# Kernel optimization log

Measured on AMD Instinct MI355X. Metric: run time of the kernel, lower is better.

Reference implementation:

```python
import jax, jax.numpy as jnp
import numpy as np

H = 1024      # hidden_size
I = 2048      # intermediate_size
E = 32        # num_routed_experts
B, S = 4, 2048


def setup_inputs() -> dict:
    key = jax.random.key(0)
    ks = jax.random.split(key, 8)
    scale = 0.02
    inp = {
        "hidden_states": jax.random.normal(ks[0], (B, S, H), dtype=jnp.float32),
        # router gate: stored [H, E] so logits = x @ gate_w
        "gate_w": jax.random.normal(ks[1], (H, E), dtype=jnp.float32) * scale,
        # shared SwiGLU (num_shared_experts=1), weights stored [in, out]
        "shared_gate_w": jax.random.normal(ks[2], (H, I), dtype=jnp.float32) * scale,
        "shared_up_w": jax.random.normal(ks[3], (H, I), dtype=jnp.float32) * scale,
        "shared_down_w": jax.random.normal(ks[4], (I, H), dtype=jnp.float32) * scale,
        # routed grouped SwiGLU, weights stored [E, in, out] (matches GroupedLinear)
        "routed_gate_w": jax.random.normal(ks[5], (E, H, I), dtype=jnp.float32) * scale,
        "routed_up_w": jax.random.normal(ks[6], (E, H, I), dtype=jnp.float32) * scale,
        "routed_down_w": jax.random.normal(ks[7], (E, I, H), dtype=jnp.float32) * scale,
    }
    return inp


def _grouped_mm(a, w, group_sizes):
    # a: [T, in], w: [E, in, out], group_sizes: [E] int32 -> [T, out]
    return jax.lax.ragged_dot(a, w, group_sizes)


def _swiglu(x, gw, uw, dw):
    return (jax.nn.silu(x @ gw) * (x @ uw)) @ dw


def reference(hidden_states, gate_w, shared_gate_w, shared_up_w, shared_down_w,
              routed_gate_w, routed_up_w, routed_down_w):
    b, s, h = hidden_states.shape
    x = hidden_states.reshape(-1, h)                      # [T, H]

    # ---- shared expert ----
    shared_out = _swiglu(x, shared_gate_w, shared_up_w, shared_down_w)

    # ---- router: top-1 ----
    logits = x @ gate_w                                   # [T, E]
    topk_ids = jnp.argmax(logits, axis=-1)                # [T]
    topk_val = jnp.max(logits, axis=-1)                   # [T]
    scores = jax.nn.sigmoid(topk_val)[:, None]            # [T, 1]
    xs = x * scores                                       # scale tokens by router score

    # ---- dispatch: sort tokens by expert id ----
    tokens_per_expert = jnp.zeros((E,), jnp.int32).at[topk_ids].add(1)
    order = jnp.argsort(topk_ids)                         # token ids sorted by expert
    sorted_x = xs[order]                                  # [T, H]

    # ---- grouped SwiGLU experts ----
    g = _grouped_mm(sorted_x, routed_gate_w, tokens_per_expert)   # [T, I]
    u = _grouped_mm(sorted_x, routed_up_w, tokens_per_expert)     # [T, I]
    d = _grouped_mm(jax.nn.silu(g) * u, routed_down_w, tokens_per_expert)  # [T, H]

    # ---- combine: unsort back to token order ----
    inv = jnp.argsort(order)
    routed_out = d[inv]

    return (shared_out + routed_out).reshape(b, s, h)
```

## Files before the change

### kernel.cpp

```cpp
#include <hip/hip_runtime.h>
#include <stdint.h>
#include <stddef.h>

#define TOK 8192
#define H 1024
#define IDIM 2048
#define NE 32
#define BM 128
#define BK 64
#define MAX_TILES 96
#define GUTILES (TOK / BM + MAX_TILES)
#define DNCONV_TILES 16896
#define RT_BLOCKS (TOK / 8)
#define GUCONV_TILES 33792

typedef __attribute__((ext_vector_type(8))) short short8;
typedef __attribute__((ext_vector_type(4))) float f32x4;
typedef __attribute__((ext_vector_type(4))) float float4v;
typedef __attribute__((ext_vector_type(4))) unsigned int uint4v;


__device__ __forceinline__ unsigned short f2bf(float x) {
  unsigned u = __builtin_bit_cast(unsigned, x);
  u += 0x7fffu + ((u >> 16) & 1u);
  return (unsigned short)(u >> 16);
}

__device__ __forceinline__ unsigned cvtpk(float lo, float hi) {
  unsigned r;
  asm("v_cvt_pk_bf16_f32 %0, %1, %2" : "=v"(r) : "v"(lo), "v"(hi));
  return r;
}

__device__ __forceinline__ void gll16(const void* g, void* l) {
  __builtin_amdgcn_global_load_lds(
      (const __attribute__((address_space(1))) unsigned int*)g,
      (__attribute__((address_space(3))) unsigned int*)l, 16, 0, 0);
}

__device__ __forceinline__ f32x4 mfma16(short8 a, short8 b, f32x4 c) {
  return __builtin_amdgcn_mfma_f32_16x16x32_bf16(a, b, c, 0, 0, 0);
}

__device__ __forceinline__ void tconv_tile(
    const float* __restrict__ src, unsigned short* __restrict__ dst,
    int K, int N, int k0, int n0, int tid, void* smem)
{
  float (*t)[65] = (float(*)[65])smem;
  {
    const int r = tid >> 4;
    const int c = (tid & 15) * 4;
    #pragma unroll
    for (int i = 0; i < 4; ++i) {
      float4v v = *(const float4v*)(src + (size_t)(k0 + r + i * 16) * N + (n0 + c));
      t[r + i * 16][c + 0] = v[0];
      t[r + i * 16][c + 1] = v[1];
      t[r + i * 16][c + 2] = v[2];
      t[r + i * 16][c + 3] = v[3];
    }
  }
  __syncthreads();
  {
    const int n = tid >> 2;
    const int kc = (tid & 3) * 16;
    uint4v o0, o1;
    #pragma unroll
    for (int q = 0; q < 4; ++q) {
      o0[q] = cvtpk(t[kc + 2 * q][n],     t[kc + 2 * q + 1][n]);
      o1[q] = cvtpk(t[kc + 8 + 2 * q][n], t[kc + 8 + 2 * q + 1][n]);
    }
    unsigned short* dp = dst + (size_t)(n0 + n) * K + (k0 + kc);
    *(uint4v*)dp = o0;
    *(uint4v*)(dp + 8) = o1;
  }
}


__global__ __launch_bounds__(256) void router_tconv_kernel(
    const float* __restrict__ x, const float* __restrict__ gw,
    unsigned short* __restrict__ xbf, unsigned short* __restrict__ xsbf,
    int* __restrict__ expert_id, int* __restrict__ counts,
    const float* __restrict__ sgw, const float* __restrict__ suw,
    const float* __restrict__ rgw, const float* __restrict__ ruw,
    unsigned short* __restrict__ sgwT, unsigned short* __restrict__ suwT,
    unsigned short* __restrict__ rgwT, unsigned short* __restrict__ ruwT)
{
  __shared__ char smem[41088];
  const int tid = threadIdx.x;
  const int b = blockIdx.x;

  if (b >= RT_BLOCKS) {
    const int flat = b - RT_BLOCKS;
    const float* src;
    unsigned short* dst;
    int rem;
    if (flat < 512 * NE) {
      const int e = flat >> 9; rem = flat & 511;
      src = rgw + (size_t)e * H * IDIM; dst = rgwT + (size_t)e * H * IDIM;
    } else if (flat < 1024 * NE) {
      const int e = (flat - 512 * NE) >> 9; rem = flat & 511;
      src = ruw + (size_t)e * H * IDIM; dst = ruwT + (size_t)e * H * IDIM;
    } else if (flat < 1024 * NE + 512) {
      rem = flat - 1024 * NE;
      src = sgw; dst = sgwT;
    } else {
      rem = flat - 1024 * NE - 512;
      src = suw; dst = suwT;
    }
    tconv_tile(src, dst, H, IDIM, (rem >> 5) * 64, (rem & 31) * 64, tid, smem);
    return;
  }

  float* xl = (float*)smem;
  float (*plog)[8][NE] = (float(*)[8][NE])(smem + 32768);
  float* sscore = (float*)(smem + 40960);
  const long t0 = (long)b * 8;

  const float4v* src = (const float4v*)(x + t0 * H);
  float4v* dst = (float4v*)xl;
  #pragma unroll
  for (int i = 0; i < 8; ++i) dst[tid + i * 256] = src[tid + i * 256];
  __syncthreads();

  {
    const int e = tid & 31, c = tid >> 5;
    float acc[8] = {0, 0, 0, 0, 0, 0, 0, 0};
    const float* gp = gw + (c * 128) * NE + e;
    for (int h = 0; h < 128; ++h) {
      float g = gp[h * NE];
      const float* xr = xl + (c * 128 + h);
      #pragma unroll
      for (int tk = 0; tk < 8; ++tk) acc[tk] += xr[tk * H] * g;
    }
    #pragma unroll
    for (int tk = 0; tk < 8; ++tk) plog[c][tk][e] = acc[tk];
  }
  __syncthreads();
  {
    const int e = tid & 31, tok = tid >> 5;
    float lg = 0.f;
    #pragma unroll
    for (int c = 0; c < 8; ++c) lg += plog[c][tok][e];
    float m = lg; int be = e;
    #pragma unroll
    for (int mask = 16; mask >= 1; mask >>= 1) {
      float om = __shfl_xor(m, mask);
      int   oe = __shfl_xor(be, mask);
      if (om > m || (om == m && oe < be)) { m = om; be = oe; }
    }
    if (e == 0) {
      sscore[tok] = 1.f / (1.f + __expf(-m));
      expert_id[t0 + tok] = be;
      atomicAdd(&counts[be], 1);
    }
  }
  __syncthreads();
  {
    const float sc = sscore[tid >> 5];
    const int base = (tid >> 5) * H + (tid & 31) * 32;
    #pragma unroll
    for (int i = 0; i < 4; ++i) {
      uint4v vx, vs;
      #pragma unroll
      for (int q = 0; q < 4; ++q) {
        const float a = xl[base + i * 8 + 2 * q];
        const float bq = xl[base + i * 8 + 2 * q + 1];
        vx[q] = cvtpk(a, bq);
        vs[q] = cvtpk(a * sc, bq * sc);
      }
      *(uint4v*)(xbf  + t0 * H + base + i * 8) = vx;
      *(uint4v*)(xsbf + t0 * H + base + i * 8) = vs;
    }
  }
}


__global__ void scan_kernel(const int* __restrict__ counts, int* __restrict__ offsets,
                            int* __restrict__ cursor, int* __restrict__ tile_e,
                            int* __restrict__ tile_p, int* __restrict__ n_tiles)
{
  if (threadIdx.x != 0) return;
  int off = 0, nt = 0;
  for (int e = 0; e < NE; ++e) {
    offsets[e] = off; cursor[e] = off;
    int cc = counts[e];
    for (int k = 0; k < cc; k += BM) { tile_e[nt] = e; tile_p[nt] = off + k; ++nt; }
    off += cc;
  }
  offsets[NE] = off;
  n_tiles[0] = nt;
}


__global__ __launch_bounds__(256) void perm_kernel(
    const int* __restrict__ expert_id, int* __restrict__ cursor, int* __restrict__ perm)
{
  int t = blockIdx.x * 256 + threadIdx.x;
  int e = expert_id[t];
  int pos = atomicAdd(&cursor[e], 1);
  perm[pos] = t;
}


__global__ __launch_bounds__(256, 2) void gu_kernel(
    const unsigned short* __restrict__ xbf,
    const unsigned short* __restrict__ xsbf,
    const unsigned short* __restrict__ SG, const unsigned short* __restrict__ SU,
    const unsigned short* __restrict__ RG, const unsigned short* __restrict__ RU,
    unsigned short* __restrict__ act_sh, unsigned short* __restrict__ act_rt,
    const float* __restrict__ SDW, const float* __restrict__ RDW,
    unsigned short* __restrict__ SDT, unsigned short* __restrict__ RDT,
    const int* __restrict__ perm, const int* __restrict__ tile_e,
    const int* __restrict__ tile_p, const int* __restrict__ offsets,
    const int* __restrict__ n_tiles)
{
  __shared__ char smem[49152];

  const int tid = threadIdx.x;
  const int bidy = blockIdx.y;

  if (bidy >= GUTILES) {
    const int flat = (bidy - GUTILES) * (int)gridDim.x + (int)blockIdx.x;
    const float* src;
    unsigned short* dst;
    int rem;
    if (flat < 512 * NE) {
      const int e = flat >> 9;
      rem = flat & 511;
      src = RDW + (size_t)e * IDIM * H;
      dst = RDT + (size_t)e * IDIM * H;
    } else {
      rem = flat - 512 * NE;
      src = SDW;
      dst = SDT;
    }
    tconv_tile(src, dst, IDIM, H, (rem >> 4) * 64, (rem & 15) * 64, tid, smem);
    return;
  }

  short* Al = (short*)smem;
  short* Gl = Al + BM * BK;
  short* Ul = Gl + 128 * BK;

  const int wave = tid >> 6, lane = tid & 63;
  const int wm = wave >> 1, wn = wave & 1;

  const bool routed = bidy >= (TOK / BM);
  int row0, row_end;
  const unsigned short *Gt, *Ut, *A;
  unsigned short* act;
  if (routed) {
    const int tx = bidy - TOK / BM;
    if (tx >= *n_tiles) return;
    const int e = tile_e[tx];
    row0 = tile_p[tx];
    row_end = offsets[e + 1];
    Gt = RG + (size_t)e * H * IDIM;
    Ut = RU + (size_t)e * H * IDIM;
    A = xsbf; act = act_rt;
  } else {
    row0 = bidy * BM; row_end = row0 + BM;
    Gt = SG; Ut = SU;
    A = xbf; act = act_sh;
  }
  const int n0 = blockIdx.x * 128;

  const unsigned short *asrc[4], *gsrc[4], *usrc[4];
  int soff[4];
  #pragma unroll
  for (int i = 0; i < 4; ++i) {
    const int r = wave * 32 + i * 8 + (lane >> 3);
    int p = row0 + r;
    if (routed && p >= row_end) p = row0;
    const int arow = routed ? perm[p] : p;
    const int cb = ((lane & 7) * 16) ^ ((r & 7) << 4);
    asrc[i] = A  + (size_t)arow * H + (cb >> 1);
    gsrc[i] = Gt + (size_t)(n0 + r) * H + (cb >> 1);
    usrc[i] = Ut + (size_t)(n0 + r) * H + (cb >> 1);
    soff[i] = (wave * 32 + i * 8) * BK;
  }

  f32x4 accg[4][4] = {};
  f32x4 accu[4][4] = {};

  #pragma unroll 1
  for (int kt = 0; kt < H / BK; ++kt) {
    __syncthreads();
    #pragma unroll
    for (int i = 0; i < 4; ++i) gll16(asrc[i] + kt * BK, Al + soff[i]);
    #pragma unroll
    for (int i = 0; i < 4; ++i) gll16(gsrc[i] + kt * BK, Gl + soff[i]);
    #pragma unroll
    for (int i = 0; i < 4; ++i) gll16(usrc[i] + kt * BK, Ul + soff[i]);
    __syncthreads();

    #pragma unroll
    for (int kk = 0; kk < 2; ++kk) {
      short8 af[4];
      #pragma unroll
      for (int m = 0; m < 4; ++m) {
        const int r = wm * 64 + m * 16 + (lane & 15);
        const int cb = (kk * 64 + ((lane >> 4) * 16)) ^ ((r & 7) << 4);
        af[m] = *(const short8*)((const char*)Al + r * 128 + cb);
      }
      #pragma unroll
      for (int nf = 0; nf < 4; ++nf) {
        const int n = wn * 64 + nf * 16 + (lane & 15);
        const int cb = (kk * 64 + ((lane >> 4) * 16)) ^ ((n & 7) << 4);
        short8 bg = *(const short8*)((const char*)Gl + n * 128 + cb);
        short8 bu = *(const short8*)((const char*)Ul + n * 128 + cb);
        #pragma unroll
        for (int m = 0; m < 4; ++m) {
          accg[m][nf] = mfma16(af[m], bg, accg[m][nf]);
          accu[m][nf] = mfma16(af[m], bu, accu[m][nf]);
        }
      }
    }
  }

  #pragma unroll
  for (int m = 0; m < 4; ++m)
    #pragma unroll
    for (int nf = 0; nf < 4; ++nf) {
      const int col = n0 + wn * 64 + nf * 16 + (lane & 15);
      #pragma unroll
      for (int j = 0; j < 4; ++j) {
        const int row = row0 + wm * 64 + m * 16 + ((lane >> 4) * 4) + j;
        if (routed && row >= row_end) continue;
        const float g = accg[m][nf][j];
        const float u = accu[m][nf][j];
        const float v = (g / (1.f + __expf(-g))) * u;
        act[(size_t)row * IDIM + col] = f2bf(v);
      }
    }
}


__global__ __launch_bounds__(256, 4) void dn_kernel(
    const unsigned short* __restrict__ act_sh,
    const unsigned short* __restrict__ act_rt,
    const unsigned short* __restrict__ SD, const unsigned short* __restrict__ RD,
    float* __restrict__ out, float* __restrict__ out_rt,
    const int* __restrict__ perm, const int* __restrict__ tile_e,
    const int* __restrict__ tile_p, const int* __restrict__ offsets,
    const int* __restrict__ n_tiles)
{
  __shared__ short Al[BM * BK];
  __shared__ short Dl[128 * BK];

  const int tid = threadIdx.x;
  const int wave = tid >> 6, lane = tid & 63;
  const int wm = wave >> 1, wn = wave & 1;

  const int bidy = blockIdx.y;
  const bool routed = bidy >= (TOK / BM);
  int row0, row_end;
  const unsigned short *Dt, *A;
  if (routed) {
    const int tx = bidy - TOK / BM;
    if (tx >= *n_tiles) return;
    const int e = tile_e[tx];
    row0 = tile_p[tx];
    row_end = offsets[e + 1];
    Dt = RD + (size_t)e * H * IDIM;
    A = act_rt;
  } else {
    row0 = bidy * BM; row_end = row0 + BM;
    Dt = SD;
    A = act_sh;
  }
  const int n0 = blockIdx.x * 128;

  const unsigned short *asrc[4], *dsrc[4];
  int soff[4];
  #pragma unroll
  for (int i = 0; i < 4; ++i) {
    const int r = wave * 32 + i * 8 + (lane >> 3);
    int p = row0 + r;
    if (routed && p >= row_end) p = row0;
    const int cb = ((lane & 7) * 16) ^ ((r & 7) << 4);
    asrc[i] = A  + (size_t)p * IDIM + (cb >> 1);
    dsrc[i] = Dt + (size_t)(n0 + r) * IDIM + (cb >> 1);
    soff[i] = (wave * 32 + i * 8) * BK;
  }

  f32x4 acc[4][4] = {};

  #pragma unroll 1
  for (int kt = 0; kt < IDIM / BK; ++kt) {
    __syncthreads();
    #pragma unroll
    for (int i = 0; i < 4; ++i) gll16(asrc[i] + kt * BK, Al + soff[i]);
    #pragma unroll
    for (int i = 0; i < 4; ++i) gll16(dsrc[i] + kt * BK, Dl + soff[i]);
    __syncthreads();

    #pragma unroll
    for (int kk = 0; kk < 2; ++kk) {
      short8 af[4];
      #pragma unroll
      for (int m = 0; m < 4; ++m) {
        const int r = wm * 64 + m * 16 + (lane & 15);
        const int cb = (kk * 64 + ((lane >> 4) * 16)) ^ ((r & 7) << 4);
        af[m] = *(const short8*)((const char*)Al + r * 128 + cb);
      }
      #pragma unroll
      for (int nf = 0; nf < 4; ++nf) {
        const int n = wn * 64 + nf * 16 + (lane & 15);
        const int cb = (kk * 64 + ((lane >> 4) * 16)) ^ ((n & 7) << 4);
        short8 bd = *(const short8*)((const char*)Dl + n * 128 + cb);
        #pragma unroll
        for (int m = 0; m < 4; ++m) acc[m][nf] = mfma16(af[m], bd, acc[m][nf]);
      }
    }
  }

  #pragma unroll
  for (int m = 0; m < 4; ++m)
    #pragma unroll
    for (int nf = 0; nf < 4; ++nf) {
      const int col = n0 + wn * 64 + nf * 16 + (lane & 15);
      #pragma unroll
      for (int j = 0; j < 4; ++j) {
        const int row = row0 + wm * 64 + m * 16 + ((lane >> 4) * 4) + j;
        if (routed && row >= row_end) continue;
        const float v = acc[m][nf][j];
        if (routed) {
          const int t = perm[row];
          out_rt[(size_t)t * H + col] = v;
        } else {
          out[(size_t)row * H + col] = v;
        }
      }
    }
}


__global__ __launch_bounds__(256) void combine_kernel(
    float* __restrict__ out, const float* __restrict__ out_rt)
{
  const size_t i = ((size_t)blockIdx.x * 256 + threadIdx.x) * 4;
  float4v a = *(float4v*)(out + i);
  float4v b = *(const float4v*)(out_rt + i);
  a[0] += b[0]; a[1] += b[1]; a[2] += b[2]; a[3] += b[3];
  *(float4v*)(out + i) = a;
}


extern "C" void kernel_launch(void* const* d_in, const int* in_sizes, int n_in,
                              void* d_out, int out_size, void* d_ws, size_t ws_size,
                              hipStream_t stream) {
  (void)in_sizes; (void)n_in; (void)out_size; (void)ws_size;
  const float* x      = (const float*)d_in[0];
  const float* gate_w = (const float*)d_in[1];
  const float* sgw    = (const float*)d_in[2];
  const float* suw    = (const float*)d_in[3];
  const float* sdw    = (const float*)d_in[4];
  const float* rgw    = (const float*)d_in[5];
  const float* ruw    = (const float*)d_in[6];
  const float* rdw    = (const float*)d_in[7];
  float* out = (float*)d_out;

  char* ws = (char*)d_ws;
  unsigned short* xbf    = (unsigned short*)(ws + 0);
  unsigned short* xsbf   = (unsigned short*)(ws + 16777216);
  unsigned short* act_sh = (unsigned short*)(ws + 33554432);
  int* perm      = (int*)(ws + 67108864);
  int* expert_id = (int*)(ws + 67141632);
  int* counts    = (int*)(ws + 67174400);
  int* offsets   = (int*)(ws + 67174528);
  int* cursor    = (int*)(ws + 67174784);
  int* tile_e    = (int*)(ws + 67174912);
  int* tile_p    = (int*)(ws + 67175424);
  int* n_tiles   = (int*)(ws + 67175936);
  unsigned short* rgwT   = (unsigned short*)(ws + 68157440);
  unsigned short* ruwT   = (unsigned short*)(ws + 202375168);
  unsigned short* rdwT   = (unsigned short*)(ws + 336592896);
  unsigned short* sgwT   = (unsigned short*)(ws + 470810624);
  unsigned short* suwT   = (unsigned short*)(ws + 475004928);
  unsigned short* sdwT   = (unsigned short*)(ws + 479199232);
  unsigned short* act_rt = (unsigned short*)(ws + 483393536);
  float*          out_rt = (float*)(ws + 516947968);

  hipMemsetAsync(counts, 0, NE * sizeof(int), stream);

  router_tconv_kernel<<<RT_BLOCKS + GUCONV_TILES, 256, 0, stream>>>(
      x, gate_w, xbf, xsbf, expert_id, counts,
      sgw, suw, rgw, ruw, sgwT, suwT, rgwT, ruwT);
  scan_kernel<<<1, 64, 0, stream>>>(counts, offsets, cursor, tile_e, tile_p, n_tiles);
  perm_kernel<<<TOK / 256, 256, 0, stream>>>(expert_id, cursor, perm);

  gu_kernel<<<dim3(IDIM / 128, GUTILES + DNCONV_TILES / (IDIM / 128)), 256, 0, stream>>>(
      xbf, xsbf, sgwT, suwT, rgwT, ruwT, act_sh, act_rt,
      sdw, rdw, sdwT, rdwT,
      perm, tile_e, tile_p, offsets, n_tiles);

  dn_kernel<<<dim3(H / 128, TOK / BM + MAX_TILES), 256, 0, stream>>>(
      act_sh, act_rt, sdwT, rdwT, out, out_rt,
      perm, tile_e, tile_p, offsets, n_tiles);
  combine_kernel<<<TOK * H / 1024, 256, 0, stream>>>(out, out_rt);
}
```

Baseline: 597.9 us.

## Split gate/up and down GEMMs into staged kernels overlapping shared and routed work

Restructures the expert pipeline into three kernels. The first runs the routed gate/up GEMM together with the down-weight conversion. The second co-schedules the shared gate/up GEMM with the routed down GEMM. The third runs the shared down GEMM alone. GEMM bodies are factored into shared device functions. The aim is better load balance and less tail idle time by pairing independent shared and routed work in the same launch. The cost is an extra kernel launch and many idle blocks in guB, since the routed-down part uses only 8 of 16 x-blocks.

```diff
diff --git a/kernel.cpp b/kernel.cpp
--- a/kernel.cpp
+++ b/kernel.cpp
@@ -9,7 +9,7 @@
 #define BM 128
 #define BK 64
 #define MAX_TILES 96
-#define GUTILES (TOK / BM + MAX_TILES)
+#define SH_TILES (TOK / BM)
 #define DNCONV_TILES 16896
 #define RT_BLOCKS (TOK / 8)
 #define GUCONV_TILES 33792
@@ -73,6 +73,163 @@
     *(uint4v*)dp = o0;
     *(uint4v*)(dp + 8) = o1;
   }
+}
+
+
+__device__ __forceinline__ void gu_tile(
+    const unsigned short* __restrict__ A,
+    const unsigned short* __restrict__ Gt, const unsigned short* __restrict__ Ut,
+    unsigned short* __restrict__ act, const int* __restrict__ permp,
+    int row0, int row_end, int n0, int tid, char* smem)
+{
+  short* Al = (short*)smem;
+  short* Gl = Al + BM * BK;
+  short* Ul = Gl + 128 * BK;
+
+  const int wave = tid >> 6, lane = tid & 63;
+  const int wm = wave >> 1, wn = wave & 1;
+
+  const unsigned short *asrc[4], *gsrc[4], *usrc[4];
+  int soff[4];
+  #pragma unroll
+  for (int i = 0; i < 4; ++i) {
+    const int r = wave * 32 + i * 8 + (lane >> 3);
+    int p = row0 + r;
+    if (permp && p >= row_end) p = row0;
+    const int arow = permp ? permp[p] : p;
+    const int cb = ((lane & 7) * 16) ^ ((r & 7) << 4);
+    asrc[i] = A  + (size_t)arow * H + (cb >> 1);
+    gsrc[i] = Gt + (size_t)(n0 + r) * H + (cb >> 1);
+    usrc[i] = Ut + (size_t)(n0 + r) * H + (cb >> 1);
+    soff[i] = (wave * 32 + i * 8) * BK;
+  }
+
+  f32x4 accg[4][4] = {};
+  f32x4 accu[4][4] = {};
+
+  #pragma unroll 1
+  for (int kt = 0; kt < H / BK; ++kt) {
+    __syncthreads();
+    #pragma unroll
+    for (int i = 0; i < 4; ++i) gll16(asrc[i] + kt * BK, Al + soff[i]);
+    #pragma unroll
+    for (int i = 0; i < 4; ++i) gll16(gsrc[i] + kt * BK, Gl + soff[i]);
+    #pragma unroll
+    for (int i = 0; i < 4; ++i) gll16(usrc[i] + kt * BK, Ul + soff[i]);
+    __syncthreads();
+
+    #pragma unroll
+    for (int kk = 0; kk < 2; ++kk) {
+      short8 af[4];
+      #pragma unroll
+      for (int m = 0; m < 4; ++m) {
+        const int r = wm * 64 + m * 16 + (lane & 15);
+        const int cb = (kk * 64 + ((lane >> 4) * 16)) ^ ((r & 7) << 4);
+        af[m] = *(const short8*)((const char*)Al + r * 128 + cb);
+      }
+      #pragma unroll
+      for (int nf = 0; nf < 4; ++nf) {
+        const int n = wn * 64 + nf * 16 + (lane & 15);
+        const int cb = (kk * 64 + ((lane >> 4) * 16)) ^ ((n & 7) << 4);
+        short8 bg = *(const short8*)((const char*)Gl + n * 128 + cb);
+        short8 bu = *(const short8*)((const char*)Ul + n * 128 + cb);
+        #pragma unroll
+        for (int m = 0; m < 4; ++m) {
+          accg[m][nf] = mfma16(af[m], bg, accg[m][nf]);
+          accu[m][nf] = mfma16(af[m], bu, accu[m][nf]);
+        }
+      }
+    }
+  }
+
+  #pragma unroll
+  for (int m = 0; m < 4; ++m)
+    #pragma unroll
+    for (int nf = 0; nf < 4; ++nf) {
+      const int col = n0 + wn * 64 + nf * 16 + (lane & 15);
+      #pragma unroll
+      for (int j = 0; j < 4; ++j) {
+        const int row = row0 + wm * 64 + m * 16 + ((lane >> 4) * 4) + j;
+        if (permp && row >= row_end) continue;
+        const float g = accg[m][nf][j];
+        const float u = accu[m][nf][j];
+        const float v = (g / (1.f + __expf(-g))) * u;
+        act[(size_t)row * IDIM + col] = f2bf(v);
+      }
+    }
+}
+
+
+__device__ __forceinline__ void dn_tile(
+    const unsigned short* __restrict__ A,
+    const unsigned short* __restrict__ Dt,
+    float* __restrict__ outbuf, const int* __restrict__ permp,
+    int row0, int row_end, int n0, int tid, char* smem)
+{
+  short* Al = (short*)smem;
+  short* Dl = Al + BM * BK;
+
+  const int wave = tid >> 6, lane = tid & 63;
+  const int wm = wave >> 1, wn = wave & 1;
+
+  const unsigned short *asrc[4], *dsrc[4];
+  int soff[4];
+  #pragma unroll
+  for (int i = 0; i < 4; ++i) {
+    const int r = wave * 32 + i * 8 + (lane >> 3);
+    int p = row0 + r;
+    if (permp && p >= row_end) p = row0;
+    const int cb = ((lane & 7) * 16) ^ ((r & 7) << 4);
+    asrc[i] = A  + (size_t)p * IDIM + (cb >> 1);
+    dsrc[i] = Dt + (size_t)(n0 + r) * IDIM + (cb >> 1);
+    soff[i] = (wave * 32 + i * 8) * BK;
+  }
+
+  f32x4 acc[4][4] = {};
+
+  #pragma unroll 1
+  for (int kt = 0; kt < IDIM / BK; ++kt) {
+    __syncthreads();
+    #pragma unroll
+    for (int i = 0; i < 4; ++i) gll16(asrc[i] + kt * BK, Al + soff[i]);
+    #pragma unroll
+    for (int i = 0; i < 4; ++i) gll16(dsrc[i] + kt * BK, Dl + soff[i]);
+    __syncthreads();
+
+    #pragma unroll
+    for (int kk = 0; kk < 2; ++kk) {
+      short8 af[4];
+      #pragma unroll
+      for (int m = 0; m < 4; ++m) {
+        const int r = wm * 64 + m * 16 + (lane & 15);
+        const int cb = (kk * 64 + ((lane >> 4) * 16)) ^ ((r & 7) << 4);
+        af[m] = *(const short8*)((const char*)Al + r * 128 + cb);
+      }
+      #pragma unroll
+      for (int nf = 0; nf < 4; ++nf) {
+        const int n = wn * 64 + nf * 16 + (lane & 15);
+        const int cb = (kk * 64 + ((lane >> 4) * 16)) ^ ((n & 7) << 4);
+        short8 bd = *(const short8*)((const char*)Dl + n * 128 + cb);
+        #pragma unroll
+        for (int m = 0; m < 4; ++m) acc[m][nf] = mfma16(af[m], bd, acc[m][nf]);
+      }
+    }
+  }
+
+  #pragma unroll
+  for (int m = 0; m < 4; ++m)
+    #pragma unroll
+    for (int nf = 0; nf < 4; ++nf) {
+      const int col = n0 + wn * 64 + nf * 16 + (lane & 15);
+      #pragma unroll
+      for (int j = 0; j < 4; ++j) {
+        const int row = row0 + wm * 64 + m * 16 + ((lane >> 4) * 4) + j;
+        if (permp && row >= row_end) continue;
+        const float v = acc[m][nf][j];
+        const int t = permp ? permp[row] : row;
+        outbuf[(size_t)t * H + col] = v;
+      }
+    }
 }
 
 
@@ -191,7 +348,6 @@
   n_tiles[0] = nt;
 }
 
-
 __global__ __launch_bounds__(256) void perm_kernel(
     const int* __restrict__ expert_id, int* __restrict__ cursor, int* __restrict__ perm)
 {
@@ -202,12 +358,10 @@
 }
 
 
-__global__ __launch_bounds__(256, 2) void gu_kernel(
-    const unsigned short* __restrict__ xbf,
+__global__ __launch_bounds__(256, 2) void guA_kernel(
     const unsigned short* __restrict__ xsbf,
-    const unsigned short* __restrict__ SG, const unsigned short* __restrict__ SU,
     const unsigned short* __restrict__ RG, const unsigned short* __restrict__ RU,
-    unsigned short* __restrict__ act_sh, unsigned short* __restrict__ act_rt,
+    unsigned short* __restrict__ act_rt,
     const float* __restrict__ SDW, const float* __restrict__ RDW,
     unsigned short* __restrict__ SDT, unsigned short* __restrict__ RDT,
     const int* __restrict__ perm, const int* __restrict__ tile_e,
@@ -215,12 +369,11 @@
     const int* __restrict__ n_tiles)
 {
   __shared__ char smem[49152];
-
   const int tid = threadIdx.x;
   const int bidy = blockIdx.y;
 
-  if (bidy >= GUTILES) {
-    const int flat = (bidy - GUTILES) * (int)gridDim.x + (int)blockIdx.x;
+  if (bidy >= MAX_TILES) {
+    const int flat = (bidy - MAX_TILES) * (int)gridDim.x + (int)blockIdx.x;
     const float* src;
     unsigned short* dst;
     int rem;
@@ -238,201 +391,52 @@
     return;
   }
 
-  short* Al = (short*)smem;
-  short* Gl = Al + BM * BK;
-  short* Ul = Gl + 128 * BK;
-
-  const int wave = tid >> 6, lane = tid & 63;
-  const int wm = wave >> 1, wn = wave & 1;
-
-  const bool routed = bidy >= (TOK / BM);
-  int row0, row_end;
-  const unsigned short *Gt, *Ut, *A;
-  unsigned short* act;
-  if (routed) {
-    const int tx = bidy - TOK / BM;
-    if (tx >= *n_tiles) return;
-    const int e = tile_e[tx];
-    row0 = tile_p[tx];
-    row_end = offsets[e + 1];
-    Gt = RG + (size_t)e * H * IDIM;
-    Ut = RU + (size_t)e * H * IDIM;
-    A = xsbf; act = act_rt;
-  } else {
-    row0 = bidy * BM; row_end = row0 + BM;
-    Gt = SG; Ut = SU;
-    A = xbf; act = act_sh;
-  }
-  const int n0 = blockIdx.x * 128;
-
-  const unsigned short *asrc[4], *gsrc[4], *usrc[4];
-  int soff[4];
-  #pragma unroll
-  for (int i = 0; i < 4; ++i) {
-    const int r = wave * 32 + i * 8 + (lane >> 3);
-    int p = row0 + r;
-    if (routed && p >= row_end) p = row0;
-    const int arow = routed ? perm[p] : p;
-    const int cb = ((lane & 7) * 16) ^ ((r & 7) << 4);
-    asrc[i] = A  + (size_t)arow * H + (cb >> 1);
-    gsrc[i] = Gt + (size_t)(n0 + r) * H + (cb >> 1);
-    usrc[i] = Ut + (size_t)(n0 + r) * H + (cb >> 1);
-    soff[i] = (wave * 32 + i * 8) * BK;
-  }
-
-  f32x4 accg[4][4] = {};
-  f32x4 accu[4][4] = {};
-
-  #pragma unroll 1
-  for (int kt = 0; kt < H / BK; ++kt) {
-    __syncthreads();
-    #pragma unroll
-    for (int i = 0; i < 4; ++i) gll16(asrc[i] + kt * BK, Al + soff[i]);
-    #pragma unroll
-    for (int i = 0; i < 4; ++i) gll16(gsrc[i] + kt * BK, Gl + soff[i]);
-    #pragma unroll
-    for (int i = 0; i < 4; ++i) gll16(usrc[i] + kt * BK, Ul + soff[i]);
-    __syncthreads();
-
-    #pragma unroll
-    for (int kk = 0; kk < 2; ++kk) {
-      short8 af[4];
-      #pragma unroll
-      for (int m = 0; m < 4; ++m) {
-        const int r = wm * 64 + m * 16 + (lane & 15);
-        const int cb = (kk * 64 + ((lane >> 4) * 16)) ^ ((r & 7) << 4);
-        af[m] = *(const short8*)((const char*)Al + r * 128 + cb);
-      }
-      #pragma unroll
-      for (int nf = 0; nf < 4; ++nf) {
-        const int n = wn * 64 + nf * 16 + (lane & 15);
-        const int cb = (kk * 64 + ((lane >> 4) * 16)) ^ ((n & 7) << 4);
-        short8 bg = *(const short8*)((const char*)Gl + n * 128 + cb);
-        short8 bu = *(const short8*)((const char*)Ul + n * 128 + cb);
-        #pragma unroll
-        for (int m = 0; m < 4; ++m) {
-          accg[m][nf] = mfma16(af[m], bg, accg[m][nf]);
-          accu[m][nf] = mfma16(af[m], bu, accu[m][nf]);
-        }
-      }
-    }
-  }
-
-  #pragma unroll
-  for (int m = 0; m < 4; ++m)
-    #pragma unroll
-    for (int nf = 0; nf < 4; ++nf) {
-      const int col = n0 + wn * 64 + nf * 16 + (lane & 15);
-      #pragma unroll
-      for (int j = 0; j < 4; ++j) {
-        const int row = row0 + wm * 64 + m * 16 + ((lane >> 4) * 4) + j;
-        if (routed && row >= row_end) continue;
-        const float g = accg[m][nf][j];
-        const float u = accu[m][nf][j];
-        const float v = (g / (1.f + __expf(-g))) * u;
-        act[(size_t)row * IDIM + col] = f2bf(v);
-      }
-    }
-}
-
-
-__global__ __launch_bounds__(256, 4) void dn_kernel(
-    const unsigned short* __restrict__ act_sh,
+  if (bidy >= *n_tiles) return;
+  const int e = tile_e[bidy];
+  gu_tile(xsbf, RG + (size_t)e * H * IDIM, RU + (size_t)e * H * IDIM,
+          act_rt, perm, tile_p[bidy], offsets[e + 1],
+          blockIdx.x * 128, tid, smem);
+}
+
+
+__global__ __launch_bounds__(256, 2) void guB_kernel(
+    const unsigned short* __restrict__ xbf,
+    const unsigned short* __restrict__ SG, const unsigned short* __restrict__ SU,
+    unsigned short* __restrict__ act_sh,
     const unsigned short* __restrict__ act_rt,
-    const unsigned short* __restrict__ SD, const unsigned short* __restrict__ RD,
-    float* __restrict__ out, float* __restrict__ out_rt,
+    const unsigned short* __restrict__ RD,
+    float* __restrict__ out_rt,
     const int* __restrict__ perm, const int* __restrict__ tile_e,
     const int* __restrict__ tile_p, const int* __restrict__ offsets,
     const int* __restrict__ n_tiles)
 {
-  __shared__ short Al[BM * BK];
-  __shared__ short Dl[128 * BK];
-
+  __shared__ char smem[49152];
   const int tid = threadIdx.x;
-  const int wave = tid >> 6, lane = tid & 63;
-  const int wm = wave >> 1, wn = wave & 1;
-
   const int bidy = blockIdx.y;
-  const bool routed = bidy >= (TOK / BM);
-  int row0, row_end;
-  const unsigned short *Dt, *A;
-  if (routed) {
-    const int tx = bidy - TOK / BM;
-    if (tx >= *n_tiles) return;
-    const int e = tile_e[tx];
-    row0 = tile_p[tx];
-    row_end = offsets[e + 1];
-    Dt = RD + (size_t)e * H * IDIM;
-    A = act_rt;
-  } else {
-    row0 = bidy * BM; row_end = row0 + BM;
-    Dt = SD;
-    A = act_sh;
-  }
-  const int n0 = blockIdx.x * 128;
-
-  const unsigned short *asrc[4], *dsrc[4];
-  int soff[4];
-  #pragma unroll
-  for (int i = 0; i < 4; ++i) {
-    const int r = wave * 32 + i * 8 + (lane >> 3);
-    int p = row0 + r;
-    if (routed && p >= row_end) p = row0;
-    const int cb = ((lane & 7) * 16) ^ ((r & 7) << 4);
-    asrc[i] = A  + (size_t)p * IDIM + (cb >> 1);
-    dsrc[i] = Dt + (size_t)(n0 + r) * IDIM + (cb >> 1);
-    soff[i] = (wave * 32 + i * 8) * BK;
-  }
-
-  f32x4 acc[4][4] = {};
-
-  #pragma unroll 1
-  for (int kt = 0; kt < IDIM / BK; ++kt) {
-    __syncthreads();
-    #pragma unroll
-    for (int i = 0; i < 4; ++i) gll16(asrc[i] + kt * BK, Al + soff[i]);
-    #pragma unroll
-    for (int i = 0; i < 4; ++i) gll16(dsrc[i] + kt * BK, Dl + soff[i]);
-    __syncthreads();
-
-    #pragma unroll
-    for (int kk = 0; kk < 2; ++kk) {
-      short8 af[4];
-      #pragma unroll
-      for (int m = 0; m < 4; ++m) {
-        const int r = wm * 64 + m * 16 + (lane & 15);
-        const int cb = (kk * 64 + ((lane >> 4) * 16)) ^ ((r & 7) << 4);
-        af[m] = *(const short8*)((const char*)Al + r * 128 + cb);
-      }
-      #pragma unroll
-      for (int nf = 0; nf < 4; ++nf) {
-        const int n = wn * 64 + nf * 16 + (lane & 15);
-        const int cb = (kk * 64 + ((lane >> 4) * 16)) ^ ((n & 7) << 4);
-        short8 bd = *(const short8*)((const char*)Dl + n * 128 + cb);
-        #pragma unroll
-        for (int m = 0; m < 4; ++m) acc[m][nf] = mfma16(af[m], bd, acc[m][nf]);
-      }
-    }
-  }
-
-  #pragma unroll
-  for (int m = 0; m < 4; ++m)
-    #pragma unroll
-    for (int nf = 0; nf < 4; ++nf) {
-      const int col = n0 + wn * 64 + nf * 16 + (lane & 15);
-      #pragma unroll
-      for (int j = 0; j < 4; ++j) {
-        const int row = row0 + wm * 64 + m * 16 + ((lane >> 4) * 4) + j;
-        if (routed && row >= row_end) continue;
-        const float v = acc[m][nf][j];
-        if (routed) {
-          const int t = perm[row];
-          out_rt[(size_t)t * H + col] = v;
-        } else {
-          out[(size_t)row * H + col] = v;
-        }
-      }
-    }
+
+  if (bidy < SH_TILES) {
+    gu_tile(xbf, SG, SU, act_sh, nullptr,
+            bidy * BM, bidy * BM + BM, blockIdx.x * 128, tid, smem);
+    return;
+  }
+  if ((int)blockIdx.x >= H / 128) return;
+  const int tx = bidy - SH_TILES;
+  if (tx >= *n_tiles) return;
+  const int e = tile_e[tx];
+  dn_tile(act_rt, RD + (size_t)e * H * IDIM, out_rt, perm,
+          tile_p[tx], offsets[e + 1], blockIdx.x * 128, tid, smem);
+}
+
+
+__global__ __launch_bounds__(256, 4) void dnsh_kernel(
+    const unsigned short* __restrict__ act_sh,
+    const unsigned short* __restrict__ SD,
+    float* __restrict__ out)
+{
+  __shared__ char smem[32768];
+  dn_tile(act_sh, SD, out, nullptr,
+          blockIdx.y * BM, blockIdx.y * BM + BM, blockIdx.x * 128,
+          threadIdx.x, smem);
 }
 
 
@@ -490,13 +494,14 @@
   scan_kernel<<<1, 64, 0, stream>>>(counts, offsets, cursor, tile_e, tile_p, n_tiles);
   perm_kernel<<<TOK / 256, 256, 0, stream>>>(expert_id, cursor, perm);
 
-  gu_kernel<<<dim3(IDIM / 128, GUTILES + DNCONV_TILES / (IDIM / 128)), 256, 0, stream>>>(
-      xbf, xsbf, sgwT, suwT, rgwT, ruwT, act_sh, act_rt,
-      sdw, rdw, sdwT, rdwT,
+  guA_kernel<<<dim3(IDIM / 128, MAX_TILES + DNCONV_TILES / (IDIM / 128)), 256, 0, stream>>>(
+      xsbf, rgwT, ruwT, act_rt, sdw, rdw, sdwT, rdwT,
       perm, tile_e, tile_p, offsets, n_tiles);
 
-  dn_kernel<<<dim3(H / 128, TOK / BM + MAX_TILES), 256, 0, stream>>>(
-      act_sh, act_rt, sdwT, rdwT, out, out_rt,
+  guB_kernel<<<dim3(IDIM / 128, SH_TILES + MAX_TILES), 256, 0, stream>>>(
+      xbf, sgwT, suwT, act_sh, act_rt, rdwT, out_rt,
       perm, tile_e, tile_p, offsets, n_tiles);
+
+  dnsh_kernel<<<dim3(H / 128, TOK / BM), 256, 0, stream>>>(act_sh, sdwT, out);
   combine_kernel<<<TOK * H / 1024, 256, 0, stream>>>(out, out_rt);
 }
```

Result: slower. 665.8 us (+11.4%).
